# Optimization experiments

Measured on AMD Instinct MI355X. Metric: run time of the kernel, lower is better.

Reference implementation:

```python
import jax, jax.numpy as jnp
import numpy as np

# PQMatcher forward (cleaned): per passage timestep i, additive (Bahdanau-style)
# attention over all question positions:
#   x = tanh(Wp(Up[i]) + Wq(Uq) + Wv(v));  s = x . v;  a = softmax(s over lq)
#   c[i] = a @ Uq
# The original python loop over i is loop-invariant except Wp(Up[i]), so it
# vectorizes exactly into one broadcasted tanh + einsum. (The original also
# computed a duplicate s_/a_ from Upr==Up and Uqr==Uq which is identical math
# and unused; we compute it once.)

LP, LQ, BZ, SZ, H = 400, 50, 32, 768, 128


def setup_inputs() -> dict:
    key = jax.random.key(0)
    ks = jax.random.split(key, 9)
    s_in = 1.0 / np.sqrt(SZ)
    s_h = 1.0 / np.sqrt(H)
    return {
        "Up": jax.random.normal(ks[0], (LP, BZ, SZ), jnp.float32),
        "Uq": jax.random.normal(ks[1], (LQ, BZ, SZ), jnp.float32),
        "Wp_w": jax.random.normal(ks[2], (H, SZ), jnp.float32) * s_in,
        "Wp_b": jax.random.normal(ks[3], (H,), jnp.float32) * s_in,
        "Wq_w": jax.random.normal(ks[4], (H, SZ), jnp.float32) * s_in,
        "Wq_b": jax.random.normal(ks[5], (H,), jnp.float32) * s_in,
        "Wv_w": jax.random.normal(ks[6], (H, H), jnp.float32) * s_h,
        "Wv_b": jax.random.normal(ks[7], (H,), jnp.float32) * s_h,
        "v": jax.random.normal(ks[8], (BZ, H), jnp.float32),
    }


def reference(Up, Uq, Wp_w, Wp_b, Wq_w, Wq_b, Wv_w, Wv_b, v):
    # Projections (loop-invariant parts hoisted out of the original loop)
    Wup = jnp.einsum("pbs,hs->pbh", Up, Wp_w) + Wp_b  # [lp, bz, h]
    Wuq = jnp.einsum("qbs,hs->qbh", Uq, Wq_w) + Wq_b  # [lq, bz, h]
    Wvv = jnp.einsum("bh,gh->bg", v, Wv_w) + Wv_b      # [bz, h]
    # tanh score fusion: [lp, lq, bz, h]
    x = jnp.tanh(Wup[:, None, :, :] + Wuq[None, :, :, :] + Wvv[None, None, :, :])
    # scores s[i] = x[i] . v  -> [lp, bz, lq]
    s = jnp.einsum("pqbh,bh->pbq", x, v)
    a = jax.nn.softmax(s, axis=-1)                      # softmax over question len
    # contexts c[i] = a[i] @ Uq -> [lp, bz, sz]
    c = jnp.einsum("pbq,qbs->pbs", a, Uq)
    return c
```

## Files before the change

kernel.cpp:

```cpp
#include <hip/hip_runtime.h>

#define LP 400
#define LQ 50
#define BZ 32
#define SZ 768
#define HH 128
#define PROWS 14464

typedef unsigned short u16;
typedef __attribute__((ext_vector_type(8))) short short8;
typedef __attribute__((ext_vector_type(4))) float f32x4;

__device__ __forceinline__ float fexp2(float x) {
#if __has_builtin(__builtin_amdgcn_exp2f)
  return __builtin_amdgcn_exp2f(x);
#else
  return exp2f(x);
#endif
}
__device__ __forceinline__ float frcp(float x) {
#if __has_builtin(__builtin_amdgcn_rcpf)
  return __builtin_amdgcn_rcpf(x);
#else
  return 1.0f / x;
#endif
}

__device__ __forceinline__ unsigned pack2(float x, float y) {
  return (__float_as_uint(x) >> 16) | (__float_as_uint(y) & 0xffff0000u);
}
__device__ __forceinline__ float remf(float x) {
  return x - __uint_as_float(__float_as_uint(x) & 0xffff0000u);
}

__global__ __launch_bounds__(256) void convw_kernel(
    const float* __restrict__ Wp_w, const float* __restrict__ Wq_w,
    u16* __restrict__ Wph, u16* __restrict__ Wpl,
    u16* __restrict__ Wqh, u16* __restrict__ Wql) {
  int gid = blockIdx.x * 256 + threadIdx.x;
  int base = gid * 8;
  const float* src;
  u16 *dh, *dl;
  if (base < HH * SZ) {
    src = Wp_w + base; dh = Wph + base; dl = Wpl + base;
  } else {
    int o = base - HH * SZ;
    src = Wq_w + o; dh = Wqh + o; dl = Wql + o;
  }
  float4 x0 = *(const float4*)src;
  float4 x1 = *(const float4*)(src + 4);
  uint4 H, L;
  H.x = pack2(x0.x, x0.y); H.y = pack2(x0.z, x0.w);
  H.z = pack2(x1.x, x1.y); H.w = pack2(x1.z, x1.w);
  L.x = pack2(remf(x0.x), remf(x0.y)); L.y = pack2(remf(x0.z), remf(x0.w));
  L.z = pack2(remf(x1.x), remf(x1.y)); L.w = pack2(remf(x1.z), remf(x1.w));
  *(uint4*)dh = H;
  *(uint4*)dl = L;
}

__global__ __launch_bounds__(256) void wvv_kernel(
    const float* __restrict__ v, const float* __restrict__ Wv_w,
    const float* __restrict__ Wv_b, float* __restrict__ Wvv) {
  int id = blockIdx.x * 256 + threadIdx.x;
  int b = id >> 7, g = id & 127;
  const float4* vb = reinterpret_cast<const float4*>(v + b * HH);
  const float4* wr = reinterpret_cast<const float4*>(Wv_w + g * HH);
  float s = Wv_b[g];
#pragma unroll
  for (int i = 0; i < HH / 4; ++i) {
    float4 a = vb[i], w = wr[i];
    s = fmaf(a.x, w.x, s); s = fmaf(a.y, w.y, s);
    s = fmaf(a.z, w.z, s); s = fmaf(a.w, w.w, s);
  }
  Wvv[id] = s;
}

__global__ __launch_bounds__(256, 1) void mfma_gemm(
    const float* __restrict__ Up, const float* __restrict__ Uq,
    const u16* __restrict__ Wph, const u16* __restrict__ Wpl,
    const u16* __restrict__ Wqh, const u16* __restrict__ Wql,
    float* __restrict__ partial) {
  __shared__ u16 Ah[128][40], Al[128][40], Bh[128][40], Bl[128][40];
  const int t = threadIdx.x, lane = t & 63, wid = t >> 6;
  const int bx = blockIdx.x, z = blockIdx.y;
  const int m0 = bx * 128;
  const bool probq = (bx >= 100);
  const u16* WH = probq ? Wqh : Wph;
  const u16* WL = probq ? Wql : Wpl;
  const int k0base = z * 384;

  const int ra = t >> 1, kh = (t & 1) * 16;
  const int grow = m0 + ra;
  const float* srcA = nullptr;
  if (grow < 12800) srcA = Up + grow * SZ;
  else if (grow < 14400) srcA = Uq + (grow - 12800) * SZ;
  const u16* srcWH = WH + ra * SZ;
  const u16* srcWL = WL + ra * SZ;

  const int wm = (wid >> 1) * 64, wn = (wid & 1) * 64;
  const int fr = lane & 15, fg = lane >> 4;

  f32x4 acc[4][4];
#pragma unroll
  for (int i = 0; i < 4; ++i)
#pragma unroll
    for (int j = 0; j < 4; ++j) acc[i][j] = (f32x4){0.f, 0.f, 0.f, 0.f};

  float4 a0, a1, a2, a3;
  uint4 wh0, wh1, wl0, wl1;

#define GLOAD(s)                                                         \
  do {                                                                   \
    int kk = k0base + (s) * 32 + kh;                                     \
    if (srcA) {                                                          \
      a0 = *(const float4*)(srcA + kk);                                  \
      a1 = *(const float4*)(srcA + kk + 4);                              \
      a2 = *(const float4*)(srcA + kk + 8);                              \
      a3 = *(const float4*)(srcA + kk + 12);                             \
    } else {                                                             \
      a0 = a1 = a2 = a3 = make_float4(0.f, 0.f, 0.f, 0.f);               \
    }                                                                    \
    wh0 = *(const uint4*)(srcWH + kk); wh1 = *(const uint4*)(srcWH + kk + 8); \
    wl0 = *(const uint4*)(srcWL + kk); wl1 = *(const uint4*)(srcWL + kk + 8); \
  } while (0)

#define WSTORE()                                                          \
  do {                                                                    \
    uint4 H0, H1, L0, L1;                                                 \
    H0.x = pack2(a0.x, a0.y); H0.y = pack2(a0.z, a0.w);                   \
    H0.z = pack2(a1.x, a1.y); H0.w = pack2(a1.z, a1.w);                   \
    H1.x = pack2(a2.x, a2.y); H1.y = pack2(a2.z, a2.w);                   \
    H1.z = pack2(a3.x, a3.y); H1.w = pack2(a3.z, a3.w);                   \
    L0.x = pack2(remf(a0.x), remf(a0.y)); L0.y = pack2(remf(a0.z), remf(a0.w)); \
    L0.z = pack2(remf(a1.x), remf(a1.y)); L0.w = pack2(remf(a1.z), remf(a1.w)); \
    L1.x = pack2(remf(a2.x), remf(a2.y)); L1.y = pack2(remf(a2.z), remf(a2.w)); \
    L1.z = pack2(remf(a3.x), remf(a3.y)); L1.w = pack2(remf(a3.z), remf(a3.w)); \
    *(uint4*)&Ah[ra][kh] = H0; *(uint4*)&Ah[ra][kh + 8] = H1;             \
    *(uint4*)&Al[ra][kh] = L0; *(uint4*)&Al[ra][kh + 8] = L1;             \
    *(uint4*)&Bh[ra][kh] = wh0; *(uint4*)&Bh[ra][kh + 8] = wh1;           \
    *(uint4*)&Bl[ra][kh] = wl0; *(uint4*)&Bl[ra][kh + 8] = wl1;           \
  } while (0)

  GLOAD(0);
  WSTORE();
  __syncthreads();

  for (int s = 0; s < 12; ++s) {
    if (s < 11) GLOAD(s + 1);
    short8 ah[4], al[4], bh[4], bl[4];
#pragma unroll
    for (int i = 0; i < 4; ++i) {
      ah[i] = *(const short8*)&Ah[wm + i * 16 + fr][fg * 8];
      al[i] = *(const short8*)&Al[wm + i * 16 + fr][fg * 8];
      bh[i] = *(const short8*)&Bh[wn + i * 16 + fr][fg * 8];
      bl[i] = *(const short8*)&Bl[wn + i * 16 + fr][fg * 8];
    }
#pragma unroll
    for (int i = 0; i < 4; ++i)
#pragma unroll
      for (int j = 0; j < 4; ++j) {
        acc[i][j] = __builtin_amdgcn_mfma_f32_16x16x32_bf16(ah[i], bh[j], acc[i][j], 0, 0, 0);
        acc[i][j] = __builtin_amdgcn_mfma_f32_16x16x32_bf16(ah[i], bl[j], acc[i][j], 0, 0, 0);
        acc[i][j] = __builtin_amdgcn_mfma_f32_16x16x32_bf16(al[i], bh[j], acc[i][j], 0, 0, 0);
      }
    __syncthreads();
    if (s < 11) WSTORE();
    __syncthreads();
  }
#undef GLOAD
#undef WSTORE

  float* pz = partial + (size_t)z * (PROWS * HH);
#pragma unroll
  for (int i = 0; i < 4; ++i) {
    int r0 = m0 + wm + i * 16 + fg * 4;
#pragma unroll
    for (int j = 0; j < 4; ++j) {
      int c = wn + j * 16 + fr;
#pragma unroll
      for (int e = 0; e < 4; ++e) pz[(r0 + e) * HH + c] = acc[i][j][e];
    }
  }
}

__global__ __launch_bounds__(256) void reduce_kernel(
    const float* __restrict__ partial, const float* __restrict__ Wp_b,
    const float* __restrict__ Wq_b, const float* __restrict__ Wvv,
    float* __restrict__ WupB, float* __restrict__ W2B, float TS) {
  int idx = blockIdx.x * 256 + threadIdx.x;
  int row = idx >> 5, h = (idx & 31) * 4;
  float4 p0 = *(const float4*)&partial[(size_t)row * HH + h];
  float4 p1 = *(const float4*)&partial[(size_t)(PROWS + row) * HH + h];
  float4 r;
  if (row < 12800) {
    float4 bb = *(const float4*)&Wp_b[h];
    r.x = (p0.x + p1.x + bb.x) * TS; r.y = (p0.y + p1.y + bb.y) * TS;
    r.z = (p0.z + p1.z + bb.z) * TS; r.w = (p0.w + p1.w + bb.w) * TS;
    *(float4*)&WupB[(size_t)row * HH + h] = r;
  } else {
    int rr = row - 12800, bz = rr & 31;
    float4 bb = *(const float4*)&Wq_b[h];
    float4 wv = *(const float4*)&Wvv[bz * HH + h];
    r.x = (p0.x + p1.x + bb.x + wv.x) * TS; r.y = (p0.y + p1.y + bb.y + wv.y) * TS;
    r.z = (p0.z + p1.z + bb.z + wv.z) * TS; r.w = (p0.w + p1.w + bb.w + wv.w) * TS;
    *(float4*)&W2B[(size_t)rr * HH + h] = r;
  }
}

__global__ __launch_bounds__(256) void score_softmax(
    const float* __restrict__ WupB, const float* __restrict__ W2B,
    const float* __restrict__ v, float* __restrict__ aw, float TS) {
  const int b = blockIdx.y, pbase = blockIdx.x * 16;
  const int t = threadIdx.x, lane = t & 63, w = t >> 6;
  __shared__ float W2s[LQ][129];
  __shared__ float Wps[16][HH];
  __shared__ float vsh[HH];

  for (int f = t; f < LQ * 32; f += 256) {
    int q = f >> 5, c4 = f & 31;
    float4 x = *(const float4*)&W2B[(size_t)(q * BZ + b) * HH + c4 * 4];
    W2s[q][c4 * 4 + 0] = x.x; W2s[q][c4 * 4 + 1] = x.y;
    W2s[q][c4 * 4 + 2] = x.z; W2s[q][c4 * 4 + 3] = x.w;
  }
  for (int f = t; f < 16 * 32; f += 256) {
    int i = f >> 5, c4 = f & 31;
    *(float4*)&Wps[i][c4 * 4] =
        *(const float4*)&WupB[(size_t)((pbase + i) * BZ + b) * HH + c4 * 4];
  }
  if (t < 32) *(float4*)&vsh[t * 4] = *(const float4*)&v[b * HH + t * 4];
  __syncthreads();

  const int q = (lane < LQ) ? lane : (LQ - 1);
  const int prow = w * 4;
  float A0 = 0.f, A1 = 0.f, A2 = 0.f, A3 = 0.f;
  for (int h = 0; h < HH; h += 4) {
#pragma unroll
    for (int j = 0; j < 4; ++j) {
      float w2 = W2s[q][h + j];
      float vj = vsh[h + j];
      float r0 = frcp(fexp2(Wps[prow + 0][h + j] + w2) + 1.f);
      float r1 = frcp(fexp2(Wps[prow + 1][h + j] + w2) + 1.f);
      float r2 = frcp(fexp2(Wps[prow + 2][h + j] + w2) + 1.f);
      float r3 = frcp(fexp2(Wps[prow + 3][h + j] + w2) + 1.f);
      A0 = fmaf(vj, r0, A0); A1 = fmaf(vj, r1, A1);
      A2 = fmaf(vj, r2, A2); A3 = fmaf(vj, r3, A3);
    }
  }

#define SOFTMAX(AR, PI)                                                   \
  do {                                                                    \
    float a = (lane < LQ) ? (AR) : 1e30f;                                 \
    float mn = a;                                                         \
    mn = fminf(mn, __shfl_xor(mn, 1));  mn = fminf(mn, __shfl_xor(mn, 2)); \
    mn = fminf(mn, __shfl_xor(mn, 4));  mn = fminf(mn, __shfl_xor(mn, 8)); \
    mn = fminf(mn, __shfl_xor(mn, 16)); mn = fminf(mn, __shfl_xor(mn, 32)); \
    float e = fexp2((mn - a) * TS);         \
    float sm = e;                                                         \
    sm += __shfl_xor(sm, 1);  sm += __shfl_xor(sm, 2);                    \
    sm += __shfl_xor(sm, 4);  sm += __shfl_xor(sm, 8);                    \
    sm += __shfl_xor(sm, 16); sm += __shfl_xor(sm, 32);                   \
    float val = e * frcp(sm);                                             \
    if (lane < LQ)                                                        \
      aw[(size_t)((pbase + prow + (PI)) * BZ + b) * LQ + lane] = val;     \
  } while (0)

  SOFTMAX(A0, 0); SOFTMAX(A1, 1); SOFTMAX(A2, 2); SOFTMAX(A3, 3);
#undef SOFTMAX
}

__global__ __launch_bounds__(192) void ctx_kernel(
    const float* __restrict__ aw, const float* __restrict__ Uq,
    float* __restrict__ out) {
  const int b = blockIdx.y;
  const int pbase = blockIdx.x * 25;
  const int t = threadIdx.x;
  __shared__ float as[25][LQ];
  for (int f = t; f < 25 * LQ; f += 192) {
    int i = f / LQ, qq = f - i * LQ;
    as[i][qq] = aw[(size_t)((pbase + i) * BZ + b) * LQ + qq];
  }
  __syncthreads();
  const int s4 = t * 4;
  f32x4 acc[25];
#pragma unroll
  for (int i = 0; i < 25; ++i) acc[i] = (f32x4){0.f, 0.f, 0.f, 0.f};
  for (int qp = 0; qp < LQ; qp += 2) {
    float4 u0 = *(const float4*)&Uq[(size_t)(qp * BZ + b) * SZ + s4];
    float4 u1 = *(const float4*)&Uq[(size_t)((qp + 1) * BZ + b) * SZ + s4];
#pragma unroll
    for (int i = 0; i < 25; ++i) {
      float2 a2 = *(const float2*)&as[i][qp];
      acc[i][0] = fmaf(a2.x, u0.x, acc[i][0]); acc[i][1] = fmaf(a2.x, u0.y, acc[i][1]);
      acc[i][2] = fmaf(a2.x, u0.z, acc[i][2]); acc[i][3] = fmaf(a2.x, u0.w, acc[i][3]);
      acc[i][0] = fmaf(a2.y, u1.x, acc[i][0]); acc[i][1] = fmaf(a2.y, u1.y, acc[i][1]);
      acc[i][2] = fmaf(a2.y, u1.z, acc[i][2]); acc[i][3] = fmaf(a2.y, u1.w, acc[i][3]);
    }
  }
#pragma unroll
  for (int i = 0; i < 25; ++i) {
    float4 r = make_float4(acc[i][0], acc[i][1], acc[i][2], acc[i][3]);
    *(float4*)&out[(size_t)((pbase + i) * BZ + b) * SZ + s4] = r;
  }
}

extern "C" void kernel_launch(void* const* d_in, const int* in_sizes, int n_in,
                              void* d_out, int out_size, void* d_ws, size_t ws_size,
                              hipStream_t stream) {
  const float* Up   = (const float*)d_in[0];
  const float* Uq   = (const float*)d_in[1];
  const float* Wp_w = (const float*)d_in[2];
  const float* Wp_b = (const float*)d_in[3];
  const float* Wq_w = (const float*)d_in[4];
  const float* Wq_b = (const float*)d_in[5];
  const float* Wv_w = (const float*)d_in[6];
  const float* Wv_b = (const float*)d_in[7];
  const float* v    = (const float*)d_in[8];
  float* out = (float*)d_out;

  float* ws   = (float*)d_ws;
  float* Wvv  = ws;
  float* WupB = Wvv + BZ * HH;
  float* W2B  = WupB + LP * BZ * HH;
  float* awB  = W2B + LQ * BZ * HH;
  u16* Wph = (u16*)(awB + LP * BZ * LQ);
  u16* Wpl = Wph + HH * SZ;
  u16* Wqh = Wpl + HH * SZ;
  u16* Wql = Wqh + HH * SZ;

  float* partial = out;

  const float TS = 2.8853900817779268f;

  convw_kernel<<<dim3(96), dim3(256), 0, stream>>>(Wp_w, Wq_w, Wph, Wpl, Wqh, Wql);
  wvv_kernel<<<dim3(16), dim3(256), 0, stream>>>(v, Wv_w, Wv_b, Wvv);
  mfma_gemm<<<dim3(113, 2), dim3(256), 0, stream>>>(Up, Uq, Wph, Wpl, Wqh, Wql, partial);
  reduce_kernel<<<dim3(1800), dim3(256), 0, stream>>>(partial, Wp_b, Wq_b, Wvv, WupB, W2B, TS);
  score_softmax<<<dim3(LP / 16, BZ), dim3(256), 0, stream>>>(WupB, W2B, v, awB, TS);
  ctx_kernel<<<dim3(16, BZ), dim3(192), 0, stream>>>(awB, Uq, out);
}
```

Before: 185.7 us.

## Fuse score softmax with context GEMV and fold projection reduce into consumers

Merges the weight-conversion and Wv projection kernels into one launch. It also limits the split-K reduce to the question rows and folds the passage-row reduce plus bias into the score kernel's shared-memory load. The score kernel now keeps the softmax weights in shared memory and computes the context output directly, so the WupB and attention-weight buffers no longer round-trip through global memory and two launches disappear. In exchange, 64 of the 256 threads sit idle during the context phase, the 16-row tile gives less reuse of Uq per block than the previous 25-row tile, and partial sums move from the output buffer into workspace.

```diff
diff --git a/kernel.cpp b/kernel.cpp
--- a/kernel.cpp
+++ b/kernel.cpp
@@ -33,46 +33,47 @@
   return x - __uint_as_float(__float_as_uint(x) & 0xffff0000u);
 }
 
-__global__ __launch_bounds__(256) void convw_kernel(
+__global__ __launch_bounds__(256) void prep_kernel(
     const float* __restrict__ Wp_w, const float* __restrict__ Wq_w,
+    const float* __restrict__ v, const float* __restrict__ Wv_w,
+    const float* __restrict__ Wv_b,
     u16* __restrict__ Wph, u16* __restrict__ Wpl,
-    u16* __restrict__ Wqh, u16* __restrict__ Wql) {
-  int gid = blockIdx.x * 256 + threadIdx.x;
-  int base = gid * 8;
-  const float* src;
-  u16 *dh, *dl;
-  if (base < HH * SZ) {
-    src = Wp_w + base; dh = Wph + base; dl = Wpl + base;
+    u16* __restrict__ Wqh, u16* __restrict__ Wql, float* __restrict__ Wvv) {
+  const int bx = blockIdx.x, t = threadIdx.x;
+  if (bx < 96) {
+    int gid = bx * 256 + t;
+    int base = gid * 8;
+    const float* src;
+    u16 *dh, *dl;
+    if (base < HH * SZ) {
+      src = Wp_w + base; dh = Wph + base; dl = Wpl + base;
+    } else {
+      int o = base - HH * SZ;
+      src = Wq_w + o; dh = Wqh + o; dl = Wql + o;
+    }
+    float4 x0 = *(const float4*)src;
+    float4 x1 = *(const float4*)(src + 4);
+    uint4 H, L;
+    H.x = pack2(x0.x, x0.y); H.y = pack2(x0.z, x0.w);
+    H.z = pack2(x1.x, x1.y); H.w = pack2(x1.z, x1.w);
+    L.x = pack2(remf(x0.x), remf(x0.y)); L.y = pack2(remf(x0.z), remf(x0.w));
+    L.z = pack2(remf(x1.x), remf(x1.y)); L.w = pack2(remf(x1.z), remf(x1.w));
+    *(uint4*)dh = H;
+    *(uint4*)dl = L;
   } else {
-    int o = base - HH * SZ;
-    src = Wq_w + o; dh = Wqh + o; dl = Wql + o;
-  }
-  float4 x0 = *(const float4*)src;
-  float4 x1 = *(const float4*)(src + 4);
-  uint4 H, L;
-  H.x = pack2(x0.x, x0.y); H.y = pack2(x0.z, x0.w);
-  H.z = pack2(x1.x, x1.y); H.w = pack2(x1.z, x1.w);
-  L.x = pack2(remf(x0.x), remf(x0.y)); L.y = pack2(remf(x0.z), remf(x0.w));
-  L.z = pack2(remf(x1.x), remf(x1.y)); L.w = pack2(remf(x1.z), remf(x1.w));
-  *(uint4*)dh = H;
-  *(uint4*)dl = L;
-}
-
-__global__ __launch_bounds__(256) void wvv_kernel(
-    const float* __restrict__ v, const float* __restrict__ Wv_w,
-    const float* __restrict__ Wv_b, float* __restrict__ Wvv) {
-  int id = blockIdx.x * 256 + threadIdx.x;
-  int b = id >> 7, g = id & 127;
-  const float4* vb = reinterpret_cast<const float4*>(v + b * HH);
-  const float4* wr = reinterpret_cast<const float4*>(Wv_w + g * HH);
-  float s = Wv_b[g];
-#pragma unroll
-  for (int i = 0; i < HH / 4; ++i) {
-    float4 a = vb[i], w = wr[i];
-    s = fmaf(a.x, w.x, s); s = fmaf(a.y, w.y, s);
-    s = fmaf(a.z, w.z, s); s = fmaf(a.w, w.w, s);
-  }
-  Wvv[id] = s;
+    int id = (bx - 96) * 256 + t;
+    int b = id >> 7, g = id & 127;
+    const float4* vb = reinterpret_cast<const float4*>(v + b * HH);
+    const float4* wr = reinterpret_cast<const float4*>(Wv_w + g * HH);
+    float s = Wv_b[g];
+#pragma unroll
+    for (int i = 0; i < HH / 4; ++i) {
+      float4 a = vb[i], w = wr[i];
+      s = fmaf(a.x, w.x, s); s = fmaf(a.y, w.y, s);
+      s = fmaf(a.z, w.z, s); s = fmaf(a.w, w.w, s);
+    }
+    Wvv[id] = s;
+  }
 }
 
 __global__ __launch_bounds__(256, 1) void mfma_gemm(
@@ -183,49 +184,53 @@
   }
 }
 
-__global__ __launch_bounds__(256) void reduce_kernel(
-    const float* __restrict__ partial, const float* __restrict__ Wp_b,
-    const float* __restrict__ Wq_b, const float* __restrict__ Wvv,
-    float* __restrict__ WupB, float* __restrict__ W2B, float TS) {
+__global__ __launch_bounds__(256) void w2prep_kernel(
+    const float* __restrict__ partial, const float* __restrict__ Wq_b,
+    const float* __restrict__ Wvv, float* __restrict__ W2B, float TS) {
   int idx = blockIdx.x * 256 + threadIdx.x;
-  int row = idx >> 5, h = (idx & 31) * 4;
+  int rr = idx >> 5, h = (idx & 31) * 4;
+  int row = 12800 + rr, b = rr & 31;
   float4 p0 = *(const float4*)&partial[(size_t)row * HH + h];
   float4 p1 = *(const float4*)&partial[(size_t)(PROWS + row) * HH + h];
+  float4 bb = *(const float4*)&Wq_b[h];
+  float4 wv = *(const float4*)&Wvv[b * HH + h];
   float4 r;
-  if (row < 12800) {
-    float4 bb = *(const float4*)&Wp_b[h];
-    r.x = (p0.x + p1.x + bb.x) * TS; r.y = (p0.y + p1.y + bb.y) * TS;
-    r.z = (p0.z + p1.z + bb.z) * TS; r.w = (p0.w + p1.w + bb.w) * TS;
-    *(float4*)&WupB[(size_t)row * HH + h] = r;
-  } else {
-    int rr = row - 12800, bz = rr & 31;
-    float4 bb = *(const float4*)&Wq_b[h];
-    float4 wv = *(const float4*)&Wvv[bz * HH + h];
-    r.x = (p0.x + p1.x + bb.x + wv.x) * TS; r.y = (p0.y + p1.y + bb.y + wv.y) * TS;
-    r.z = (p0.z + p1.z + bb.z + wv.z) * TS; r.w = (p0.w + p1.w + bb.w + wv.w) * TS;
-    *(float4*)&W2B[(size_t)rr * HH + h] = r;
-  }
-}
-
-__global__ __launch_bounds__(256) void score_softmax(
-    const float* __restrict__ WupB, const float* __restrict__ W2B,
-    const float* __restrict__ v, float* __restrict__ aw, float TS) {
-  const int b = blockIdx.y, pbase = blockIdx.x * 16;
+  r.x = (p0.x + p1.x + bb.x + wv.x) * TS;
+  r.y = (p0.y + p1.y + bb.y + wv.y) * TS;
+  r.z = (p0.z + p1.z + bb.z + wv.z) * TS;
+  r.w = (p0.w + p1.w + bb.w + wv.w) * TS;
+  *(float4*)&W2B[(size_t)rr * HH + h] = r;
+}
+
+__global__ __launch_bounds__(256) void score_ctx(
+    const float* __restrict__ partial, const float* __restrict__ Wp_b,
+    const float* __restrict__ W2B, const float* __restrict__ v,
+    const float* __restrict__ Uq, float* __restrict__ out, float TS) {
+  const int f = blockIdx.x;
+  const int b = (f & 7) * 4 + ((f >> 3) & 3);
+  const int pbase = (f >> 5) * 16;
   const int t = threadIdx.x, lane = t & 63, w = t >> 6;
   __shared__ float W2s[LQ][129];
   __shared__ float Wps[16][HH];
   __shared__ float vsh[HH];
-
-  for (int f = t; f < LQ * 32; f += 256) {
-    int q = f >> 5, c4 = f & 31;
+  __shared__ float as[16][52];
+
+  for (int ff = t; ff < LQ * 32; ff += 256) {
+    int q = ff >> 5, c4 = ff & 31;
     float4 x = *(const float4*)&W2B[(size_t)(q * BZ + b) * HH + c4 * 4];
     W2s[q][c4 * 4 + 0] = x.x; W2s[q][c4 * 4 + 1] = x.y;
     W2s[q][c4 * 4 + 2] = x.z; W2s[q][c4 * 4 + 3] = x.w;
   }
-  for (int f = t; f < 16 * 32; f += 256) {
-    int i = f >> 5, c4 = f & 31;
-    *(float4*)&Wps[i][c4 * 4] =
-        *(const float4*)&WupB[(size_t)((pbase + i) * BZ + b) * HH + c4 * 4];
+  for (int ff = t; ff < 16 * 32; ff += 256) {
+    int i = ff >> 5, c4 = ff & 31;
+    int grow = (pbase + i) * BZ + b;
+    float4 p0 = *(const float4*)&partial[(size_t)grow * HH + c4 * 4];
+    float4 p1 = *(const float4*)&partial[(size_t)(PROWS + grow) * HH + c4 * 4];
+    float4 bb = *(const float4*)&Wp_b[c4 * 4];
+    float4 r;
+    r.x = (p0.x + p1.x + bb.x) * TS; r.y = (p0.y + p1.y + bb.y) * TS;
+    r.z = (p0.z + p1.z + bb.z) * TS; r.w = (p0.w + p1.w + bb.w) * TS;
+    *(float4*)&Wps[i][c4 * 4] = r;
   }
   if (t < 32) *(float4*)&vsh[t * 4] = *(const float4*)&v[b * HH + t * 4];
   __syncthreads();
@@ -260,46 +265,35 @@
     sm += __shfl_xor(sm, 4);  sm += __shfl_xor(sm, 8);                    \
     sm += __shfl_xor(sm, 16); sm += __shfl_xor(sm, 32);                   \
     float val = e * frcp(sm);                                             \
-    if (lane < LQ)                                                        \
-      aw[(size_t)((pbase + prow + (PI)) * BZ + b) * LQ + lane] = val;     \
+    if (lane < LQ) as[prow + (PI)][lane] = val;                           \
   } while (0)
 
   SOFTMAX(A0, 0); SOFTMAX(A1, 1); SOFTMAX(A2, 2); SOFTMAX(A3, 3);
 #undef SOFTMAX
-}
-
-__global__ __launch_bounds__(192) void ctx_kernel(
-    const float* __restrict__ aw, const float* __restrict__ Uq,
-    float* __restrict__ out) {
-  const int b = blockIdx.y;
-  const int pbase = blockIdx.x * 25;
-  const int t = threadIdx.x;
-  __shared__ float as[25][LQ];
-  for (int f = t; f < 25 * LQ; f += 192) {
-    int i = f / LQ, qq = f - i * LQ;
-    as[i][qq] = aw[(size_t)((pbase + i) * BZ + b) * LQ + qq];
-  }
   __syncthreads();
-  const int s4 = t * 4;
-  f32x4 acc[25];
-#pragma unroll
-  for (int i = 0; i < 25; ++i) acc[i] = (f32x4){0.f, 0.f, 0.f, 0.f};
-  for (int qp = 0; qp < LQ; qp += 2) {
-    float4 u0 = *(const float4*)&Uq[(size_t)(qp * BZ + b) * SZ + s4];
-    float4 u1 = *(const float4*)&Uq[(size_t)((qp + 1) * BZ + b) * SZ + s4];
-#pragma unroll
-    for (int i = 0; i < 25; ++i) {
-      float2 a2 = *(const float2*)&as[i][qp];
-      acc[i][0] = fmaf(a2.x, u0.x, acc[i][0]); acc[i][1] = fmaf(a2.x, u0.y, acc[i][1]);
-      acc[i][2] = fmaf(a2.x, u0.z, acc[i][2]); acc[i][3] = fmaf(a2.x, u0.w, acc[i][3]);
-      acc[i][0] = fmaf(a2.y, u1.x, acc[i][0]); acc[i][1] = fmaf(a2.y, u1.y, acc[i][1]);
-      acc[i][2] = fmaf(a2.y, u1.z, acc[i][2]); acc[i][3] = fmaf(a2.y, u1.w, acc[i][3]);
-    }
-  }
-#pragma unroll
-  for (int i = 0; i < 25; ++i) {
-    float4 r = make_float4(acc[i][0], acc[i][1], acc[i][2], acc[i][3]);
-    *(float4*)&out[(size_t)((pbase + i) * BZ + b) * SZ + s4] = r;
+
+  if (t < 192) {
+    const int s4 = t * 4;
+    f32x4 acc[16];
+#pragma unroll
+    for (int i = 0; i < 16; ++i) acc[i] = (f32x4){0.f, 0.f, 0.f, 0.f};
+    for (int qp = 0; qp < LQ; qp += 2) {
+      float4 u0 = *(const float4*)&Uq[(size_t)(qp * BZ + b) * SZ + s4];
+      float4 u1 = *(const float4*)&Uq[(size_t)((qp + 1) * BZ + b) * SZ + s4];
+#pragma unroll
+      for (int i = 0; i < 16; ++i) {
+        float2 a2 = *(const float2*)&as[i][qp];
+        acc[i][0] = fmaf(a2.x, u0.x, acc[i][0]); acc[i][1] = fmaf(a2.x, u0.y, acc[i][1]);
+        acc[i][2] = fmaf(a2.x, u0.z, acc[i][2]); acc[i][3] = fmaf(a2.x, u0.w, acc[i][3]);
+        acc[i][0] = fmaf(a2.y, u1.x, acc[i][0]); acc[i][1] = fmaf(a2.y, u1.y, acc[i][1]);
+        acc[i][2] = fmaf(a2.y, u1.z, acc[i][2]); acc[i][3] = fmaf(a2.y, u1.w, acc[i][3]);
+      }
+    }
+#pragma unroll
+    for (int i = 0; i < 16; ++i) {
+      float4 r = make_float4(acc[i][0], acc[i][1], acc[i][2], acc[i][3]);
+      *(float4*)&out[(size_t)((pbase + i) * BZ + b) * SZ + s4] = r;
+    }
   }
 }
 
@@ -317,24 +311,22 @@
   const float* v    = (const float*)d_in[8];
   float* out = (float*)d_out;
 
-  float* ws   = (float*)d_ws;
-  float* Wvv  = ws;
-  float* WupB = Wvv + BZ * HH;
-  float* W2B  = WupB + LP * BZ * HH;
-  float* awB  = W2B + LQ * BZ * HH;
-  u16* Wph = (u16*)(awB + LP * BZ * LQ);
-  u16* Wpl = Wph + HH * SZ;
-  u16* Wqh = Wpl + HH * SZ;
-  u16* Wql = Wqh + HH * SZ;
-
-  float* partial = out;
+  float* ws      = (float*)d_ws;
+  float* Wvv     = ws;
+  float* W2B     = Wvv + BZ * HH;
+  u16* Wph       = (u16*)(W2B + LQ * BZ * HH);
+  u16* Wpl       = Wph + HH * SZ;
+  u16* Wqh       = Wpl + HH * SZ;
+  u16* Wql       = Wqh + HH * SZ;
+  float* partial = (float*)(Wql + HH * SZ);
 
   const float TS = 2.8853900817779268f;
 
-  convw_kernel<<<dim3(96), dim3(256), 0, stream>>>(Wp_w, Wq_w, Wph, Wpl, Wqh, Wql);
-  wvv_kernel<<<dim3(16), dim3(256), 0, stream>>>(v, Wv_w, Wv_b, Wvv);
-  mfma_gemm<<<dim3(113, 2), dim3(256), 0, stream>>>(Up, Uq, Wph, Wpl, Wqh, Wql, partial);
-  reduce_kernel<<<dim3(1800), dim3(256), 0, stream>>>(partial, Wp_b, Wq_b, Wvv, WupB, W2B, TS);
-  score_softmax<<<dim3(LP / 16, BZ), dim3(256), 0, stream>>>(WupB, W2B, v, awB, TS);
-  ctx_kernel<<<dim3(16, BZ), dim3(192), 0, stream>>>(awB, Uq, out);
-}
+  prep_kernel<<<dim3(112), dim3(256), 0, stream>>>(
+      Wp_w, Wq_w, v, Wv_w, Wv_b, Wph, Wpl, Wqh, Wql, Wvv);
+  mfma_gemm<<<dim3(113, 2), dim3(256), 0, stream>>>(
+      Up, Uq, Wph, Wpl, Wqh, Wql, partial);
+  w2prep_kernel<<<dim3(200), dim3(256), 0, stream>>>(partial, Wq_b, Wvv, W2B, TS);
+  score_ctx<<<dim3(800), dim3(256), 0, stream>>>(
+      partial, Wp_b, W2B, v, Uq, out, TS);
+}
```

New measurement: 175.4 us. 5.5% less time.
